# Kernel optimization log

Measured on AMD Instinct MI355X. Metric: run time of the kernel, lower is better.

The kernel has to match this reference:

```python
import jax, jax.numpy as jnp
import numpy as np

B, L, U, G, H = 64, 110, 768, 512, 256
WP = WF = 10
NSP = 2
R = 2 * NSP * NSP      # 8 relation types
NB = 30                # RGCN num_bases
FF = 2048              # torch TransformerEncoderLayer default dim_feedforward
TAG = 7
N = B * L
NEG = -1e9


def _build_edges():
    # static windowed edge structure (all dialogues have length L)
    js, ks = [], []
    for j in range(L):
        for k in range(max(0, j - WP), min(L - 1, j + WF) + 1):
            js.append(j); ks.append(k)
    j = np.asarray(js, np.int32); k = np.asarray(ks, np.int32)
    c = (j >= k).astype(np.int32)  # edge_type suffix: '0' if j<k else '1'
    off = (np.arange(B, dtype=np.int32) * L)[:, None]
    src = (j[None, :] + off).reshape(-1)
    dst = (k[None, :] + off).reshape(-1)
    return src, dst, np.tile(k, B), np.tile(c, B)


def _ln(x, g, b):
    m = x.mean(-1, keepdims=True)
    v = ((x - m) ** 2).mean(-1, keepdims=True)
    return (x - m) / jnp.sqrt(v + 1e-5) * g + b


def _core(x, in_proj_w, in_proj_b, out_proj_w, out_proj_b, ln1_g, ln1_b,
          ff1_w, ff1_b, ff2_w, ff2_b, ln2_g, ln2_b, to_w, to_b, att_w,
          rgcn_basis, rgcn_comp, rgcn_root, rgcn_bias,
          gc_rel_w, gc_rel_b, gc_root_w, clf1_w, clf1_b, clf2_w, clf2_b,
          speaker, src, dst, k_local, cflag):
    # --- SeqContext: 1-layer, 1-head post-norm transformer (eval mode) ---
    qkv = x @ in_proj_w.T + in_proj_b
    q, kk, v = jnp.split(qkv, 3, axis=-1)
    attn = jax.nn.softmax(jnp.einsum('bqd,bkd->bqk', q, kk) / jnp.sqrt(jnp.float32(U)), -1)
    a = jnp.einsum('bqk,bkd->bqd', attn, v) @ out_proj_w.T + out_proj_b
    h = _ln(x + a, ln1_g, ln1_b)
    ff = jax.nn.relu(h @ ff1_w.T + ff1_b) @ ff2_w.T + ff2_b
    h = _ln(h + ff, ln2_g, ln2_b)
    feats = h @ to_w.T + to_b                      # (B, L, G) node features

    # --- EdgeAtt: windowed softmax attention, score[j,k] = x_j^T W x_k ---
    scores = jnp.einsum('bjd,de,bke->bjk', feats, att_w, feats)
    rel = jnp.arange(L)[None, :] - jnp.arange(L)[:, None]
    mask = (rel >= -WP) & (rel <= WF)
    alpha = jax.nn.softmax(jnp.where(mask[None], scores, NEG), -1)  # (B, L, L)

    xf = feats.reshape(N, G)
    edge_norm = alpha.reshape(N, L)[src, k_local]   # alpha[b, j, k] per edge

    # --- edge types from speakers: idx = (s1*NSP + s2)*2 + c ---
    sp = speaker.reshape(N)
    etype = (sp[src] * NSP + sp[dst]) * 2 + cflag

    # --- RGCNConv: basis decomposition, per-(node, relation) mean + root ---
    w_rel = jnp.einsum('rb,bgh->rgh', rgcn_comp, rgcn_basis)   # (R, G, H)
    xproj = jnp.einsum('ng,rgh->rnh', xf, w_rel)               # (R, N, H)
    msg = xproj[etype, src]                                    # (E, H)
    seg = dst * R + etype
    cnt = jax.ops.segment_sum(jnp.ones_like(edge_norm), seg, num_segments=N * R)
    msg = msg / jnp.maximum(cnt[seg], 1.0)[:, None]
    h1 = jax.ops.segment_sum(msg, dst, num_segments=N) + xf @ rgcn_root + rgcn_bias

    # --- GraphConv: sum-aggregate edge-weighted neighbors + root ---
    agg = jax.ops.segment_sum(edge_norm[:, None] * h1[src], dst, num_segments=N)
    h2 = agg @ gc_rel_w.T + gc_rel_b + h1 @ gc_root_w.T

    # --- Classifier (dropout inactive in eval) ---
    z = jnp.concatenate([xf, h2], axis=-1)
    return jax.nn.relu(z @ clf1_w.T + clf1_b) @ clf2_w.T + clf2_b  # (N, TAG)


def setup_inputs():
    key = jax.random.key(0)
    ks = jax.random.split(key, 16)
    def rn(i, shape, scale=0.02):
        return jax.random.normal(ks[i], shape, jnp.float32) * scale
    src, dst, k_local, cflag = _build_edges()
    return {
        'x': jax.random.normal(ks[0], (B, L, U), jnp.float32),
        'in_proj_w': rn(1, (3 * U, U)), 'in_proj_b': jnp.zeros((3 * U,), jnp.float32),
        'out_proj_w': rn(2, (U, U)), 'out_proj_b': jnp.zeros((U,), jnp.float32),
        'ln1_g': jnp.ones((U,), jnp.float32), 'ln1_b': jnp.zeros((U,), jnp.float32),
        'ff1_w': rn(3, (FF, U)), 'ff1_b': jnp.zeros((FF,), jnp.float32),
        'ff2_w': rn(4, (U, FF)), 'ff2_b': jnp.zeros((U,), jnp.float32),
        'ln2_g': jnp.ones((U,), jnp.float32), 'ln2_b': jnp.zeros((U,), jnp.float32),
        'to_w': rn(5, (G, U)), 'to_b': jnp.zeros((G,), jnp.float32),
        'att_w': rn(6, (G, G), 2.0 / (G + G)),
        'rgcn_basis': rn(7, (NB, G, H)), 'rgcn_comp': rn(8, (R, NB), 0.2),
        'rgcn_root': rn(9, (G, H)), 'rgcn_bias': jnp.zeros((H,), jnp.float32),
        'gc_rel_w': rn(10, (H, H)), 'gc_rel_b': jnp.zeros((H,), jnp.float32),
        'gc_root_w': rn(11, (H, H)),
        'clf1_w': rn(12, (H, G + H)), 'clf1_b': jnp.zeros((H,), jnp.float32),
        'clf2_w': rn(13, (TAG, H)), 'clf2_b': jnp.zeros((TAG,), jnp.float32),
        'speaker': jax.random.randint(ks[14], (B, L), 0, NSP, jnp.int32),
        'src': jnp.asarray(src), 'dst': jnp.asarray(dst),
        'k_local': jnp.asarray(k_local), 'cflag': jnp.asarray(cflag),
        'length': L,
    }


def reference(x, in_proj_w, in_proj_b, out_proj_w, out_proj_b, ln1_g, ln1_b,
              ff1_w, ff1_b, ff2_w, ff2_b, ln2_g, ln2_b, to_w, to_b, att_w,
              rgcn_basis, rgcn_comp, rgcn_root, rgcn_bias,
              gc_rel_w, gc_rel_b, gc_root_w, clf1_w, clf1_b, clf2_w, clf2_b,
              speaker, src, dst, k_local, cflag, length):
    return _core(x, in_proj_w, in_proj_b, out_proj_w, out_proj_b, ln1_g, ln1_b,
                 ff1_w, ff1_b, ff2_w, ff2_b, ln2_g, ln2_b, to_w, to_b, att_w,
                 rgcn_basis, rgcn_comp, rgcn_root, rgcn_bias,
                 gc_rel_w, gc_rel_b, gc_root_w, clf1_w, clf1_b, clf2_w, clf2_b,
                 speaker, src, dst, k_local, cflag)
```

## Files before the change

### kernel.cpp

```cpp
#include <hip/hip_runtime.h>
#include <hip/hip_bf16.h>
#include <math.h>

#define L_   110
#define B_   64
#define N_   7040
#define U_   768
#define G_   512
#define H_   256
#define FF_  2048
#define EPB_ 2200
#define NC_  2816

typedef __attribute__((ext_vector_type(4))) float f32x4;
typedef __attribute__((ext_vector_type(8))) short bf16x8;

__device__ __forceinline__ ushort f2b(float f) {
  union { __hip_bfloat16 h; ushort u; } cv;
  cv.h = __float2bfloat16(f);
  return cv.u;
}
__device__ __forceinline__ float b2f(ushort u) {
  union { float f; unsigned int i; } cv; cv.i = ((unsigned int)u) << 16; return cv.f;
}

__device__ __forceinline__ int edge_prefix(int j) {
  if (j <= 10)  return j * 11 + (j * (j - 1)) / 2;
  if (j <= 100) return 155 + (j - 10) * 21;
  return 2045 + ((141 - j) * (j - 100)) / 2;
}

struct Segs7 { const float* in[7]; ushort* out[7]; int n4[7]; };

__global__ __launch_bounds__(256)
void cvtmulti_kernel(Segs7 s)
{
  const int seg = blockIdx.y;
  const int n4 = s.n4[seg];
  const float* __restrict__ in = s.in[seg];
  ushort* __restrict__ out = s.out[seg];
  for (int i = blockIdx.x * 256 + threadIdx.x; i < n4; i += gridDim.x * 256) {
    float4 v = ((const float4*)in)[i];
    ushort4 o;
    o.x = f2b(v.x); o.y = f2b(v.y); o.z = f2b(v.z); o.w = f2b(v.w);
    ((ushort4*)out)[i] = o;
  }
}

__global__ __launch_bounds__(256)
void tcvt_kernel(const float* __restrict__ in, ushort* __restrict__ out,
                 int R, int C, size_t inStride, size_t outStride)
{
  __shared__ float t[32][33];
  const int bt = blockIdx.z;
  const int r0 = blockIdx.y * 32, c0 = blockIdx.x * 32;
  const int tx = threadIdx.x & 31, ty = threadIdx.x >> 5;
  for (int i = ty; i < 32; i += 8)
    t[i][tx] = in[bt * inStride + (size_t)(r0 + i) * C + c0 + tx];
  __syncthreads();
  for (int i = ty; i < 32; i += 8)
    out[bt * outStride + (size_t)(c0 + i) * R + r0 + tx] = f2b(t[tx][i]);
}

__global__ __launch_bounds__(256)
void wrel_kernel(const float* __restrict__ basis, const float* __restrict__ comp,
                 float* __restrict__ wrel)
{
  __shared__ float cs[240];
  const int tid = threadIdx.x;
  if (tid < 240) cs[tid] = comp[tid];
  __syncthreads();
  const int gh = blockIdx.x * 256 + tid;
  float acc[8] = {};
  for (int bb = 0; bb < 30; ++bb) {
    float v = basis[(size_t)bb * (G_ * H_) + gh];
#pragma unroll
    for (int r = 0; r < 8; ++r) acc[r] = fmaf(cs[r * 30 + bb], v, acc[r]);
  }
#pragma unroll
  for (int r = 0; r < 8; ++r) wrel[(size_t)r * (G_ * H_) + gh] = acc[r];
}

__global__ void biascomb_kernel(const float* __restrict__ rb, float* __restrict__ bias)
{
  int i = blockIdx.x * 256 + threadIdx.x;
  if (i < NC_) bias[i] = (i < 2560) ? 0.f : rb[i - 2560];
}

__global__ __launch_bounds__(256)
void gccat_kernel(const float* __restrict__ rel, const float* __restrict__ root,
                  ushort* __restrict__ outp)
{
  int i = blockIdx.x * 256 + threadIdx.x;
  const int r = i >> 8, c = i & 255;
  outp[(size_t)r * 512 + c]       = f2b(rel[i]);
  outp[(size_t)r * 512 + 256 + c] = f2b(root[i]);
}

template<bool BIAS, bool RELU, bool ACC, bool OUTF, bool OUTB>
__global__ __launch_bounds__(256)
void mgemm_kernel(const ushort* __restrict__ A, const ushort* __restrict__ B,
                  const float* __restrict__ bias, const float* __restrict__ Cin,
                  float* __restrict__ Cf, ushort* __restrict__ Cb,
                  int K, int lda, int ldb, int ldc)
{
  __shared__ ushort sA[128 * 64];
  __shared__ ushort sB[128 * 64];
  const int tid = threadIdx.x;
  const int w = tid >> 6, l = tid & 63;

  const int gx = gridDim.x;
  const int nwg = gx * gridDim.y;
  const int lid = blockIdx.y * gx + blockIdx.x;
  const int q = nwg >> 3, r = nwg & 7;
  const int xcd = lid & 7, pos = lid >> 3;
  const int nlid = (xcd < r ? xcd * (q + 1) : r * (q + 1) + (xcd - r) * q) + pos;
  const int m0 = (nlid / gx) * 128, n0 = (nlid % gx) * 128;

  const int srow = l >> 3, sg = l & 7, rbase = w * 32;
  const int wr = w >> 1, wc = w & 1;
  const int lrow = l & 15, lk = l >> 4;
  const int xm = (l & 7) << 4;
  const int kb0 = (lk * 16) ^ xm;
  int aoff[4], boff[4];
#pragma unroll
  for (int i = 0; i < 4; ++i) {
    aoff[i] = (wr * 64 + i * 16 + lrow) * 128 + kb0;
    boff[i] = (wc * 64 + i * 16 + lrow) * 128 + kb0;
  }

  f32x4 acc[4][4];
#pragma unroll
  for (int i = 0; i < 4; ++i)
#pragma unroll
    for (int j = 0; j < 4; ++j) acc[i][j] = (f32x4){0.f, 0.f, 0.f, 0.f};

#define STAGE(k0)                                                              \
  {                                                                            \
    _Pragma("unroll")                                                          \
    for (int i = 0; i < 4; ++i) {                                              \
      const int trow = rbase + i * 8 + srow;                                   \
      const int koff = (sg * 8) ^ ((trow & 7) << 3);                           \
      const ushort* ga = A + (size_t)(m0 + trow) * lda + (k0) + koff;          \
      const ushort* gb = B + (size_t)(n0 + trow) * ldb + (k0) + koff;          \
      __builtin_amdgcn_global_load_lds(                                        \
          (const __attribute__((address_space(1))) void*)ga,                   \
          (__attribute__((address_space(3))) void*)&sA[(rbase + i * 8) * 64],  \
          16, 0, 0);                                                           \
      __builtin_amdgcn_global_load_lds(                                        \
          (const __attribute__((address_space(1))) void*)gb,                   \
          (__attribute__((address_space(3))) void*)&sB[(rbase + i * 8) * 64],  \
          16, 0, 0);                                                           \
    }                                                                          \
  }

  STAGE(0)
  for (int kt = 0;;) {
    __syncthreads();
#pragma unroll
    for (int h = 0; h < 2; ++h) {
      const int hx = h * 64;
      bf16x8 af[4], bfr[4];
#pragma unroll
      for (int i = 0; i < 4; ++i) {
        af[i]  = *(const bf16x8*)&sA[(aoff[i] ^ hx) >> 1];
        bfr[i] = *(const bf16x8*)&sB[(boff[i] ^ hx) >> 1];
      }
#pragma unroll
      for (int mi = 0; mi < 4; ++mi)
#pragma unroll
        for (int ni = 0; ni < 4; ++ni)
          acc[mi][ni] = __builtin_amdgcn_mfma_f32_16x16x32_bf16(
              af[mi], bfr[ni], acc[mi][ni], 0, 0, 0);
    }
    kt += 64;
    if (kt >= K) break;
    __syncthreads();
    STAGE(kt)
  }
#undef STAGE

  const int orow = m0 + wr * 64 + lk * 4;
  const int ocol = n0 + wc * 64 + lrow;
#pragma unroll
  for (int mi = 0; mi < 4; ++mi) {
#pragma unroll
    for (int r2 = 0; r2 < 4; ++r2) {
      const int row = orow + mi * 16 + r2;
#pragma unroll
      for (int ni = 0; ni < 4; ++ni) {
        const int col = ocol + ni * 16;
        float v = acc[mi][ni][r2];
        if constexpr (ACC)  v += Cin[(size_t)row * ldc + col];
        if constexpr (BIAS) v += bias[col];
        if constexpr (RELU) v = fmaxf(v, 0.f);
        if constexpr (OUTF) Cf[(size_t)row * ldc + col] = v;
        if constexpr (OUTB) Cb[(size_t)row * ldc + col] = f2b(v);
      }
    }
  }
}

__global__ __launch_bounds__(256)
void vtrans_kernel(const ushort* __restrict__ qkvb, ushort* __restrict__ vt)
{
  __shared__ ushort t[32][33];
  const int b = blockIdx.z;
  const int r0 = blockIdx.y * 32;
  const int c0 = blockIdx.x * 32;
  const int tx = threadIdx.x & 31, ty = threadIdx.x >> 5;
  for (int i = ty; i < 32; i += 8) {
    const int r = r0 + i;
    t[i][tx] = (r < L_) ? qkvb[((size_t)(b * L_) + r) * 2304 + 1536 + c0 + tx]
                        : (ushort)0;
  }
  __syncthreads();
  for (int i = ty; i < 32; i += 8)
    vt[((size_t)b * 768 + c0 + i) * 128 + r0 + tx] = t[tx][i];
}

__global__ __launch_bounds__(256)
void attnM_kernel(const ushort* __restrict__ qkvb, const ushort* __restrict__ vt,
                  ushort* __restrict__ ctxb)
{
  const int wg = blockIdx.x;
  const int xcd = wg & 7, slot = wg >> 3;
  const int b = xcd * 8 + slot / 7;
  const int qr0 = (slot % 7) * 16;
  const int tid = threadIdx.x, w = tid >> 6, l = tid & 63;
  __shared__ float  sS[16 * 128];
  __shared__ ushort sP[16 * 128];
  const int lrow = l & 15, lq = l >> 4;

  const ushort* Qbase = qkvb + ((size_t)(b * L_) + qr0 + lrow) * 2304 + lq * 8;
  f32x4 accS[2] = {{0.f,0.f,0.f,0.f},{0.f,0.f,0.f,0.f}};
  const int nf0 = w * 2;
  for (int k0 = 0; k0 < 768; k0 += 32) {
    bf16x8 aq = *(const bf16x8*)(Qbase + k0);
#pragma unroll
    for (int f = 0; f < 2; ++f) {
      const int nf = nf0 + f;
      if (nf < 7) {
        const ushort* Kp = qkvb + ((size_t)(b * L_) + nf * 16 + lrow) * 2304
                         + 768 + k0 + lq * 8;
        bf16x8 bk = *(const bf16x8*)Kp;
        accS[f] = __builtin_amdgcn_mfma_f32_16x16x32_bf16(aq, bk, accS[f], 0, 0, 0);
      }
    }
  }
  const float scale = 0.03608439182435161f;
#pragma unroll
  for (int f = 0; f < 2; ++f) {
    const int nf = nf0 + f;
    if (nf < 7) {
#pragma unroll
      for (int r = 0; r < 4; ++r)
        sS[(lq * 4 + r) * 128 + nf * 16 + lrow] = accS[f][r] * scale;
    }
  }
  __syncthreads();

  {
    const int row = w * 4 + lq;
    const int c0 = lrow;
    float m = -1e30f;
    for (int c = c0; c < L_; c += 16) m = fmaxf(m, sS[row * 128 + c]);
#pragma unroll
    for (int off = 8; off; off >>= 1) m = fmaxf(m, __shfl_xor(m, off));
    float pv[7];
    float sum = 0.f;
#pragma unroll
    for (int i = 0; i < 7; ++i) {
      const int c = c0 + i * 16;
      float e = (c < L_) ? __expf(sS[row * 128 + c] - m) : 0.f;
      pv[i] = e; sum += e;
    }
#pragma unroll
    for (int off = 8; off; off >>= 1) sum += __shfl_xor(sum, off);
    const float inv = 1.f / sum;
#pragma unroll
    for (int i = 0; i < 8; ++i) {
      const int c = c0 + i * 16;
      ushort pb = (i < 7 && c < L_) ? f2b(pv[i < 7 ? i : 0] * inv) : (ushort)0;
      const int g = (c >> 3) ^ (row & 7);
      sP[row * 128 + g * 8 + (c & 7)] = pb;
    }
  }
  __syncthreads();

  f32x4 accO[12];
#pragma unroll
  for (int i = 0; i < 12; ++i) accO[i] = (f32x4){0.f, 0.f, 0.f, 0.f};
#pragma unroll
  for (int ks = 0; ks < 4; ++ks) {
    const int k = ks * 32 + lq * 8;
    const int g = (k >> 3) ^ (lrow & 7);
    bf16x8 ap = *(const bf16x8*)&sP[lrow * 128 + g * 8];
#pragma unroll
    for (int i = 0; i < 12; ++i) {
      const int col = w * 192 + i * 16 + lrow;
      bf16x8 bv = *(const bf16x8*)(vt + ((size_t)b * 768 + col) * 128 + k);
      accO[i] = __builtin_amdgcn_mfma_f32_16x16x32_bf16(ap, bv, accO[i], 0, 0, 0);
    }
  }
#pragma unroll
  for (int i = 0; i < 12; ++i) {
    const int col = w * 192 + i * 16 + lrow;
#pragma unroll
    for (int r = 0; r < 4; ++r) {
      const int row = qr0 + lq * 4 + r;
      if (row < L_)
        ctxb[((size_t)b * L_ + row) * 768 + col] = f2b(accO[i][r]);
    }
  }
}

__global__ __launch_bounds__(256)
void ln_kernel(const float* __restrict__ A, const float* __restrict__ Bres,
               const float* __restrict__ g, const float* __restrict__ beta,
               float* __restrict__ out, ushort* __restrict__ outb)
{
  const int row = blockIdx.x, tid = threadIdx.x;
  const float* ap = A + (size_t)row * U_;
  const float* bp = Bres + (size_t)row * U_;
  float v0 = ap[tid] + bp[tid];
  float v1 = ap[tid + 256] + bp[tid + 256];
  float v2 = ap[tid + 512] + bp[tid + 512];
  float s = v0 + v1 + v2, sq = v0 * v0 + v1 * v1 + v2 * v2;
  __shared__ float red[8];
#pragma unroll
  for (int off = 32; off; off >>= 1) { s += __shfl_xor(s, off); sq += __shfl_xor(sq, off); }
  const int wave = tid >> 6, lane = tid & 63;
  if (lane == 0) { red[wave] = s; red[4 + wave] = sq; }
  __syncthreads();
  if (tid == 0) {
    float ts = red[0] + red[1] + red[2] + red[3];
    float tq = red[4] + red[5] + red[6] + red[7];
    float m = ts * (1.f / 768.f);
    float var = tq * (1.f / 768.f) - m * m;
    red[0] = m; red[1] = 1.f / sqrtf(var + 1e-5f);
  }
  __syncthreads();
  const float m = red[0], inv = red[1];
  float* op = out + (size_t)row * U_;
  ushort* ob = outb + (size_t)row * U_;
  float o0 = (v0 - m) * inv * g[tid] + beta[tid];
  float o1 = (v1 - m) * inv * g[tid + 256] + beta[tid + 256];
  float o2 = (v2 - m) * inv * g[tid + 512] + beta[tid + 512];
  op[tid] = o0; op[tid + 256] = o1; op[tid + 512] = o2;
  ob[tid] = f2b(o0); ob[tid + 256] = f2b(o1); ob[tid + 512] = f2b(o2);
}

__global__ __launch_bounds__(256)
void edgeatt_kernel(const ushort* __restrict__ tmpB, const ushort* __restrict__ fcat,
                    float* __restrict__ edge_norm)
{
  const int bj = blockIdx.x;
  const int b = bj / L_, j = bj - b * L_;
  const int k0 = max(0, j - 10), k1 = min(L_ - 1, j + 10);
  __shared__ float s[32];
  const int tid = threadIdx.x;
  const int wave = tid >> 6, lane = tid & 63;
  const ushort* tp = tmpB + (size_t)bj * NC_ + lane * 8;
  float tr[8];
  {
    bf16x8 tv = *(const bf16x8*)tp;
#pragma unroll
    for (int i = 0; i < 8; ++i) tr[i] = b2f((ushort)tv[i]);
  }
  for (int k = k0 + wave; k <= k1; k += 4) {
    const ushort* fp = fcat + (size_t)(b * L_ + k) * 768 + lane * 8;
    bf16x8 v = *(const bf16x8*)fp;
    float sc = 0.f;
#pragma unroll
    for (int i = 0; i < 8; ++i) sc = fmaf(b2f((ushort)v[i]), tr[i], sc);
#pragma unroll
    for (int off = 32; off; off >>= 1) sc += __shfl_xor(sc, off);
    if (lane == 0) s[k - k0] = sc;
  }
  __syncthreads();
  if (tid == 0) {
    const int W = k1 - k0 + 1;
    float m = -1e30f;
    for (int t = 0; t < W; ++t) m = fmaxf(m, s[t]);
    float sum = 0.f;
    for (int t = 0; t < W; ++t) { float e = __expf(s[t] - m); s[t] = e; sum += e; }
    const float inv = 1.f / sum;
    const int base = b * EPB_ + edge_prefix(j);
    for (int t = 0; t < W; ++t) edge_norm[base + t] = s[t] * inv;
  }
}

__global__ __launch_bounds__(256)
void rgcn_gather2_kernel(const ushort* __restrict__ xcomb,
                         const int* __restrict__ speaker,
                         ushort* __restrict__ catb)
{
  const int tid = threadIdx.x;
  const int n = blockIdx.x * 8 + (tid >> 5);
  const int lane = tid & 31;
  const int b = n / L_, k = n - b * L_;
  const int j0 = max(0, k - 10), j1 = min(L_ - 1, k + 10);
  const int spk = speaker[n];
  float inv[4];
  {
    int cn[4] = {0, 0, 0, 0};
    for (int j = j0; j <= j1; ++j)
      cn[speaker[b * L_ + j] * 2 + (j >= k ? 1 : 0)]++;
#pragma unroll
    for (int q = 0; q < 4; ++q) inv[q] = cn[q] ? 1.f / (float)cn[q] : 0.f;
  }
  float acc[8] = {};
  for (int j = j0; j <= j1; ++j) {
    const int spj = speaker[b * L_ + j];
    const int c = (j >= k) ? 1 : 0;
    const int et = (spj * 2 + spk) * 2 + c;
    const float w = inv[spj * 2 + c];
    bf16x8 v = *(const bf16x8*)&xcomb[(size_t)(b * L_ + j) * NC_ + 512 + et * 256 + lane * 8];
#pragma unroll
    for (int i = 0; i < 8; ++i) acc[i] = fmaf(b2f((ushort)v[i]), w, acc[i]);
  }
  bf16x8 rt = *(const bf16x8*)&xcomb[(size_t)n * NC_ + 2560 + lane * 8];
  bf16x8 o;
#pragma unroll
  for (int i = 0; i < 8; ++i) o[i] = (short)f2b(acc[i] + b2f((ushort)rt[i]));
  *(bf16x8*)&catb[(size_t)n * 512 + 256 + lane * 8] = o;
}

__global__ __launch_bounds__(256)
void gcn_gather2_kernel(const float* __restrict__ edge_norm,
                        ushort* __restrict__ catb)
{
  const int tid = threadIdx.x;
  const int n = blockIdx.x * 8 + (tid >> 5);
  const int lane = tid & 31;
  const int b = n / L_, k = n - b * L_;
  const int j0 = max(0, k - 10), j1 = min(L_ - 1, k + 10);
  float acc[8] = {};
  for (int j = j0; j <= j1; ++j) {
    const float w = edge_norm[b * EPB_ + edge_prefix(j) + (k - max(0, j - 10))];
    bf16x8 v = *(const bf16x8*)&catb[(size_t)(b * L_ + j) * 512 + 256 + lane * 8];
#pragma unroll
    for (int i = 0; i < 8; ++i) acc[i] = fmaf(b2f((ushort)v[i]), w, acc[i]);
  }
  bf16x8 o;
#pragma unroll
  for (int i = 0; i < 8; ++i) o[i] = (short)f2b(acc[i]);
  *(bf16x8*)&catb[(size_t)n * 512 + lane * 8] = o;
}

__global__ __launch_bounds__(256)
void clf2_kernel(const float* __restrict__ hid, const float* __restrict__ w,
                 const float* __restrict__ bias, float* __restrict__ out)
{
  __shared__ float wsm[7 * H_];
  const int tid = threadIdx.x;
  for (int i = tid; i < 7 * H_; i += 256) wsm[i] = w[i];
  __syncthreads();
  const int idx = blockIdx.x * 256 + threadIdx.x;
  if (idx < N_ * 7) {
    const int n = idx / 7, t = idx - n * 7;
    const float* hp = hid + (size_t)n * H_;
    const float* wp = wsm + t * H_;
    float acc = bias[t];
    for (int d = 0; d < H_; ++d) acc = fmaf(hp[d], wp[d], acc);
    out[idx] = acc;
  }
}

extern "C" void kernel_launch(void* const* d_in, const int* in_sizes, int n_in,
                              void* d_out, int out_size, void* d_ws, size_t ws_size,
                              hipStream_t stream)
{
  const float* x          = (const float*)d_in[0];
  const float* in_proj_w  = (const float*)d_in[1];
  const float* in_proj_b  = (const float*)d_in[2];
  const float* out_proj_w = (const float*)d_in[3];
  const float* out_proj_b = (const float*)d_in[4];
  const float* ln1_g      = (const float*)d_in[5];
  const float* ln1_b      = (const float*)d_in[6];
  const float* ff1_w      = (const float*)d_in[7];
  const float* ff1_b      = (const float*)d_in[8];
  const float* ff2_w      = (const float*)d_in[9];
  const float* ff2_b      = (const float*)d_in[10];
  const float* ln2_g      = (const float*)d_in[11];
  const float* ln2_b      = (const float*)d_in[12];
  const float* to_w       = (const float*)d_in[13];
  const float* to_b       = (const float*)d_in[14];
  const float* att_w      = (const float*)d_in[15];
  const float* rgcn_basis = (const float*)d_in[16];
  const float* rgcn_comp  = (const float*)d_in[17];
  const float* rgcn_root  = (const float*)d_in[18];
  const float* rgcn_bias  = (const float*)d_in[19];
  const float* gc_rel_w   = (const float*)d_in[20];
  const float* gc_rel_b   = (const float*)d_in[21];
  const float* gc_root_w  = (const float*)d_in[22];
  const float* clf1_w     = (const float*)d_in[23];
  const float* clf1_b     = (const float*)d_in[24];
  const float* clf2_w     = (const float*)d_in[25];
  const float* clf2_b     = (const float*)d_in[26];
  const int*   speaker    = (const int*)d_in[27];
  float* out = (float*)d_out;
  char* p = (char*)d_ws;

  float*  R1f    = (float*)p;
  ushort* R1b    = (ushort*)p;
  p += (size_t)N_ * 2304 * 4;
  float*  aproj = (float*)p;
  float*  ffo   = aproj;
  float*  en    = (float*)(p + (size_t)N_ * 512 * 4);
  p += (size_t)N_ * 768 * 4;
  float*  hbuf  = (float*)p;
  ushort* vt    = (ushort*)p;
  float*  hid   = (float*)p;
  p += (size_t)N_ * 768 * 4;
  ushort* xb    = (ushort*)p;
  ushort* ctxb  = xb;
  p += (size_t)N_ * 768 * 2;
  ushort* hb    = (ushort*)p;
  ushort* catb  = hb;
  p += (size_t)N_ * 768 * 2;
  ushort* fcat  = (ushort*)p; p += (size_t)N_ * 768 * 2;
  ushort* in_projb = (ushort*)p; p += (size_t)2304 * 768 * 2;
  ushort* out_projb= (ushort*)p; p += (size_t)768 * 768 * 2;
  ushort* ff1b     = (ushort*)p; p += (size_t)2048 * 768 * 2;
  ushort* ff2b     = (ushort*)p; p += (size_t)768 * 2048 * 2;
  ushort* tob      = (ushort*)p; p += (size_t)512 * 768 * 2;
  ushort* combw    = (ushort*)p; p += (size_t)NC_ * 512 * 2;
  ushort* gccat    = (ushort*)p; p += (size_t)256 * 512 * 2;
  ushort* clf1b16  = (ushort*)p; p += (size_t)256 * 768 * 2;
  float*  bias_comb= (float*)p;  p += NC_ * 4;
  float*  wrelTmp  = R1f;

  Segs7 segs;
  segs.in[0] = x;          segs.out[0] = xb;        segs.n4[0] = N_ * 768 / 4;
  segs.in[1] = in_proj_w;  segs.out[1] = in_projb;  segs.n4[1] = 2304 * 768 / 4;
  segs.in[2] = out_proj_w; segs.out[2] = out_projb; segs.n4[2] = 768 * 768 / 4;
  segs.in[3] = ff1_w;      segs.out[3] = ff1b;      segs.n4[3] = 2048 * 768 / 4;
  segs.in[4] = ff2_w;      segs.out[4] = ff2b;      segs.n4[4] = 768 * 2048 / 4;
  segs.in[5] = to_w;       segs.out[5] = tob;       segs.n4[5] = 512 * 768 / 4;
  segs.in[6] = clf1_w;     segs.out[6] = clf1b16;   segs.n4[6] = 256 * 768 / 4;
  cvtmulti_kernel<<<dim3(768, 7), 256, 0, stream>>>(segs);
  gccat_kernel<<<256, 256, 0, stream>>>(gc_rel_w, gc_root_w, gccat);
  tcvt_kernel<<<dim3(16, 16, 1), 256, 0, stream>>>(att_w, combw, 512, 512, 0, 0);
  wrel_kernel<<<512, 256, 0, stream>>>(rgcn_basis, rgcn_comp, wrelTmp);
  tcvt_kernel<<<dim3(8, 16, 8), 256, 0, stream>>>(wrelTmp, combw + (size_t)512 * 512,
                                                  512, 256,
                                                  (size_t)512 * 256, (size_t)256 * 512);
  tcvt_kernel<<<dim3(8, 16, 1), 256, 0, stream>>>(rgcn_root, combw + (size_t)2560 * 512,
                                                  512, 256, 0, 0);
  biascomb_kernel<<<11, 256, 0, stream>>>(rgcn_bias, bias_comb);

  mgemm_kernel<true, false, false, false, true><<<dim3(18, 55), 256, 0, stream>>>(
      xb, in_projb, in_proj_b, nullptr, nullptr, R1b, 768, 768, 768, 2304);
  vtrans_kernel<<<dim3(24, 4, 64), 256, 0, stream>>>(R1b, vt);
  attnM_kernel<<<448, 256, 0, stream>>>(R1b, vt, ctxb);
  mgemm_kernel<true, false, false, true, false><<<dim3(6, 55), 256, 0, stream>>>(
      ctxb, out_projb, out_proj_b, nullptr, aproj, nullptr, 768, 768, 768, 768);
  ln_kernel<<<N_, 256, 0, stream>>>(x, aproj, ln1_g, ln1_b, hbuf, hb);
  mgemm_kernel<true, true, false, false, true><<<dim3(16, 55), 256, 0, stream>>>(
      hb, ff1b, ff1_b, nullptr, nullptr, R1b, 768, 768, 768, 2048);
  mgemm_kernel<true, false, false, true, false><<<dim3(6, 55), 256, 0, stream>>>(
      R1b, ff2b, ff2_b, nullptr, ffo, nullptr, 2048, 2048, 2048, 768);
  ln_kernel<<<N_, 256, 0, stream>>>(hbuf, ffo, ln2_g, ln2_b, hbuf, hb);
  mgemm_kernel<true, false, false, false, true><<<dim3(4, 55), 256, 0, stream>>>(
      hb, tob, to_b, nullptr, nullptr, fcat, 768, 768, 768, 768);
  mgemm_kernel<true, false, false, false, true><<<dim3(22, 55), 256, 0, stream>>>(
      fcat, combw, bias_comb, nullptr, nullptr, R1b, 512, 768, 512, NC_);
  edgeatt_kernel<<<N_, 256, 0, stream>>>(R1b, fcat, en);
  rgcn_gather2_kernel<<<N_ / 8, 256, 0, stream>>>(R1b, speaker, catb);
  gcn_gather2_kernel<<<N_ / 8, 256, 0, stream>>>(en, catb);
  mgemm_kernel<true, false, false, false, true><<<dim3(2, 55), 256, 0, stream>>>(
      catb, gccat, gc_rel_b, nullptr, nullptr, fcat + 512, 512, 512, 512, 768);
  mgemm_kernel<true, true, false, true, false><<<dim3(2, 55), 256, 0, stream>>>(
      fcat, clf1b16, clf1_b, nullptr, hid, nullptr, 768, 768, 768, 256);
  clf2_kernel<<<(N_ * 7 + 255) / 256, 256, 0, stream>>>(hid, clf2_w, clf2_b, out);
}
```

Measured before the change: 349.3 us.

## Fuse V-transpose into QKV GEMM, merge small kernels, switch intermediates to bf16

Several independent changes are combined. The V transpose is folded into the QKV GEMM epilogue, and the bias-combine, gccat and vt-padding-zero kernels are merged into one prep kernel. The edge-attention and RGCN gather kernels are merged into one launch, and GEMM outputs feeding LayerNorm and clf2 are stored as bf16 instead of fp32. The aim is to cut launch count and memory traffic, at the cost of more rounding error and strided scattered writes for the transposed V.

New measurement: 337.1 us. -3.5%, faster.

```diff
diff --git a/kernel.cpp b/kernel.cpp
--- a/kernel.cpp
+++ b/kernel.cpp
@@ -81,27 +81,31 @@
   for (int r = 0; r < 8; ++r) wrel[(size_t)r * (G_ * H_) + gh] = acc[r];
 }
 
-__global__ void biascomb_kernel(const float* __restrict__ rb, float* __restrict__ bias)
-{
-  int i = blockIdx.x * 256 + threadIdx.x;
-  if (i < NC_) bias[i] = (i < 2560) ? 0.f : rb[i - 2560];
-}
-
-__global__ __launch_bounds__(256)
-void gccat_kernel(const float* __restrict__ rel, const float* __restrict__ root,
-                  ushort* __restrict__ outp)
-{
-  int i = blockIdx.x * 256 + threadIdx.x;
-  const int r = i >> 8, c = i & 255;
-  outp[(size_t)r * 512 + c]       = f2b(rel[i]);
-  outp[(size_t)r * 512 + 256 + c] = f2b(root[i]);
-}
-
-template<bool BIAS, bool RELU, bool ACC, bool OUTF, bool OUTB>
+__global__ __launch_bounds__(256)
+void prepmisc_kernel(const float* __restrict__ rb, const float* __restrict__ rel,
+                     const float* __restrict__ root, float* __restrict__ bias,
+                     ushort* __restrict__ gccat, ushort* __restrict__ vt)
+{
+  const int i = blockIdx.x * 256 + threadIdx.x;
+  if (i < NC_) {
+    bias[i] = (i < 2560) ? 0.f : rb[i - 2560];
+  } else if (i < NC_ + 65536) {
+    const int j = i - NC_;
+    const int r = j >> 8, c = j & 255;
+    gccat[(size_t)r * 512 + c]       = f2b(rel[j]);
+    gccat[(size_t)r * 512 + 256 + c] = f2b(root[j]);
+  } else if (i < NC_ + 65536 + 64 * 768 * 18) {
+    const int j = i - (NC_ + 65536);
+    const int bd = j / 18, kk = 110 + (j - bd * 18);
+    vt[(size_t)bd * 128 + kk] = 0;
+  }
+}
+
+template<bool BIAS, bool RELU, bool OUTB, bool VTOUT>
 __global__ __launch_bounds__(256)
 void mgemm_kernel(const ushort* __restrict__ A, const ushort* __restrict__ B,
-                  const float* __restrict__ bias, const float* __restrict__ Cin,
-                  float* __restrict__ Cf, ushort* __restrict__ Cb,
+                  const float* __restrict__ bias, ushort* __restrict__ Cb,
+                  ushort* __restrict__ Vt,
                   int K, int lda, int ldb, int ldc)
 {
   __shared__ ushort sA[128 * 64];
@@ -191,32 +195,19 @@
       for (int ni = 0; ni < 4; ++ni) {
         const int col = ocol + ni * 16;
         float v = acc[mi][ni][r2];
-        if constexpr (ACC)  v += Cin[(size_t)row * ldc + col];
         if constexpr (BIAS) v += bias[col];
         if constexpr (RELU) v = fmaxf(v, 0.f);
-        if constexpr (OUTF) Cf[(size_t)row * ldc + col] = v;
-        if constexpr (OUTB) Cb[(size_t)row * ldc + col] = f2b(v);
+        const ushort vb = f2b(v);
+        if constexpr (OUTB) Cb[(size_t)row * ldc + col] = vb;
+        if constexpr (VTOUT) {
+          if (col >= 1536) {
+            const int brow = row / L_, kk = row - brow * L_;
+            Vt[((size_t)brow * 768 + (col - 1536)) * 128 + kk] = vb;
+          }
+        }
       }
     }
   }
-}
-
-__global__ __launch_bounds__(256)
-void vtrans_kernel(const ushort* __restrict__ qkvb, ushort* __restrict__ vt)
-{
-  __shared__ ushort t[32][33];
-  const int b = blockIdx.z;
-  const int r0 = blockIdx.y * 32;
-  const int c0 = blockIdx.x * 32;
-  const int tx = threadIdx.x & 31, ty = threadIdx.x >> 5;
-  for (int i = ty; i < 32; i += 8) {
-    const int r = r0 + i;
-    t[i][tx] = (r < L_) ? qkvb[((size_t)(b * L_) + r) * 2304 + 1536 + c0 + tx]
-                        : (ushort)0;
-  }
-  __syncthreads();
-  for (int i = ty; i < 32; i += 8)
-    vt[((size_t)b * 768 + c0 + i) * 128 + r0 + tx] = t[tx][i];
 }
 
 __global__ __launch_bounds__(256)
@@ -315,17 +306,18 @@
   }
 }
 
-__global__ __launch_bounds__(256)
-void ln_kernel(const float* __restrict__ A, const float* __restrict__ Bres,
+template<bool WF>
+__global__ __launch_bounds__(256)
+void ln_kernel(const float* __restrict__ A, const ushort* __restrict__ Bres,
                const float* __restrict__ g, const float* __restrict__ beta,
                float* __restrict__ out, ushort* __restrict__ outb)
 {
   const int row = blockIdx.x, tid = threadIdx.x;
   const float* ap = A + (size_t)row * U_;
-  const float* bp = Bres + (size_t)row * U_;
-  float v0 = ap[tid] + bp[tid];
-  float v1 = ap[tid + 256] + bp[tid + 256];
-  float v2 = ap[tid + 512] + bp[tid + 512];
+  const ushort* bp = Bres + (size_t)row * U_;
+  float v0 = ap[tid] + b2f(bp[tid]);
+  float v1 = ap[tid + 256] + b2f(bp[tid + 256]);
+  float v2 = ap[tid + 512] + b2f(bp[tid + 512]);
   float s = v0 + v1 + v2, sq = v0 * v0 + v1 * v1 + v2 * v2;
   __shared__ float red[8];
 #pragma unroll
@@ -342,89 +334,85 @@
   }
   __syncthreads();
   const float m = red[0], inv = red[1];
-  float* op = out + (size_t)row * U_;
   ushort* ob = outb + (size_t)row * U_;
   float o0 = (v0 - m) * inv * g[tid] + beta[tid];
   float o1 = (v1 - m) * inv * g[tid + 256] + beta[tid + 256];
   float o2 = (v2 - m) * inv * g[tid + 512] + beta[tid + 512];
-  op[tid] = o0; op[tid + 256] = o1; op[tid + 512] = o2;
+  if constexpr (WF) {
+    float* op = out + (size_t)row * U_;
+    op[tid] = o0; op[tid + 256] = o1; op[tid + 512] = o2;
+  }
   ob[tid] = f2b(o0); ob[tid + 256] = f2b(o1); ob[tid + 512] = f2b(o2);
 }
 
 __global__ __launch_bounds__(256)
-void edgeatt_kernel(const ushort* __restrict__ tmpB, const ushort* __restrict__ fcat,
-                    float* __restrict__ edge_norm)
-{
-  const int bj = blockIdx.x;
-  const int b = bj / L_, j = bj - b * L_;
-  const int k0 = max(0, j - 10), k1 = min(L_ - 1, j + 10);
-  __shared__ float s[32];
+void graphfront_kernel(const ushort* __restrict__ combo, const ushort* __restrict__ fcat,
+                       const int* __restrict__ speaker,
+                       ushort* __restrict__ catb, float* __restrict__ edge_norm)
+{
   const int tid = threadIdx.x;
-  const int wave = tid >> 6, lane = tid & 63;
-  const ushort* tp = tmpB + (size_t)bj * NC_ + lane * 8;
-  float tr[8];
-  {
-    bf16x8 tv = *(const bf16x8*)tp;
-#pragma unroll
-    for (int i = 0; i < 8; ++i) tr[i] = b2f((ushort)tv[i]);
-  }
-  for (int k = k0 + wave; k <= k1; k += 4) {
-    const ushort* fp = fcat + (size_t)(b * L_ + k) * 768 + lane * 8;
-    bf16x8 v = *(const bf16x8*)fp;
-    float sc = 0.f;
-#pragma unroll
-    for (int i = 0; i < 8; ++i) sc = fmaf(b2f((ushort)v[i]), tr[i], sc);
-#pragma unroll
-    for (int off = 32; off; off >>= 1) sc += __shfl_xor(sc, off);
-    if (lane == 0) s[k - k0] = sc;
-  }
-  __syncthreads();
-  if (tid == 0) {
-    const int W = k1 - k0 + 1;
-    float m = -1e30f;
-    for (int t = 0; t < W; ++t) m = fmaxf(m, s[t]);
-    float sum = 0.f;
-    for (int t = 0; t < W; ++t) { float e = __expf(s[t] - m); s[t] = e; sum += e; }
-    const float inv = 1.f / sum;
-    const int base = b * EPB_ + edge_prefix(j);
-    for (int t = 0; t < W; ++t) edge_norm[base + t] = s[t] * inv;
-  }
-}
-
-__global__ __launch_bounds__(256)
-void rgcn_gather2_kernel(const ushort* __restrict__ xcomb,
-                         const int* __restrict__ speaker,
-                         ushort* __restrict__ catb)
-{
-  const int tid = threadIdx.x;
-  const int n = blockIdx.x * 8 + (tid >> 5);
-  const int lane = tid & 31;
-  const int b = n / L_, k = n - b * L_;
-  const int j0 = max(0, k - 10), j1 = min(L_ - 1, k + 10);
-  const int spk = speaker[n];
-  float inv[4];
-  {
-    int cn[4] = {0, 0, 0, 0};
-    for (int j = j0; j <= j1; ++j)
-      cn[speaker[b * L_ + j] * 2 + (j >= k ? 1 : 0)]++;
-#pragma unroll
-    for (int q = 0; q < 4; ++q) inv[q] = cn[q] ? 1.f / (float)cn[q] : 0.f;
-  }
-  float acc[8] = {};
-  for (int j = j0; j <= j1; ++j) {
-    const int spj = speaker[b * L_ + j];
-    const int c = (j >= k) ? 1 : 0;
-    const int et = (spj * 2 + spk) * 2 + c;
-    const float w = inv[spj * 2 + c];
-    bf16x8 v = *(const bf16x8*)&xcomb[(size_t)(b * L_ + j) * NC_ + 512 + et * 256 + lane * 8];
-#pragma unroll
-    for (int i = 0; i < 8; ++i) acc[i] = fmaf(b2f((ushort)v[i]), w, acc[i]);
-  }
-  bf16x8 rt = *(const bf16x8*)&xcomb[(size_t)n * NC_ + 2560 + lane * 8];
-  bf16x8 o;
-#pragma unroll
-  for (int i = 0; i < 8; ++i) o[i] = (short)f2b(acc[i] + b2f((ushort)rt[i]));
-  *(bf16x8*)&catb[(size_t)n * 512 + 256 + lane * 8] = o;
+  if (blockIdx.x < N_ / 8) {
+    const int n = blockIdx.x * 8 + (tid >> 5);
+    const int lane = tid & 31;
+    const int b = n / L_, k = n - b * L_;
+    const int j0 = max(0, k - 10), j1 = min(L_ - 1, k + 10);
+    const int spk = speaker[n];
+    float inv[4];
+    {
+      int cn[4] = {0, 0, 0, 0};
+      for (int j = j0; j <= j1; ++j)
+        cn[speaker[b * L_ + j] * 2 + (j >= k ? 1 : 0)]++;
+#pragma unroll
+      for (int q = 0; q < 4; ++q) inv[q] = cn[q] ? 1.f / (float)cn[q] : 0.f;
+    }
+    float acc[8] = {};
+    for (int j = j0; j <= j1; ++j) {
+      const int spj = speaker[b * L_ + j];
+      const int c = (j >= k) ? 1 : 0;
+      const int et = (spj * 2 + spk) * 2 + c;
+      const float w = inv[spj * 2 + c];
+      bf16x8 v = *(const bf16x8*)&combo[(size_t)(b * L_ + j) * NC_ + 512 + et * 256 + lane * 8];
+#pragma unroll
+      for (int i = 0; i < 8; ++i) acc[i] = fmaf(b2f((ushort)v[i]), w, acc[i]);
+    }
+    bf16x8 rt = *(const bf16x8*)&combo[(size_t)n * NC_ + 2560 + lane * 8];
+    bf16x8 o;
+#pragma unroll
+    for (int i = 0; i < 8; ++i) o[i] = (short)f2b(acc[i] + b2f((ushort)rt[i]));
+    *(bf16x8*)&catb[(size_t)n * 512 + 256 + lane * 8] = o;
+  } else {
+    const int bj = blockIdx.x - N_ / 8;
+    const int b = bj / L_, j = bj - b * L_;
+    const int k0 = max(0, j - 10), k1 = min(L_ - 1, j + 10);
+    __shared__ float s[32];
+    const int wave = tid >> 6, lane = tid & 63;
+    float tr[8];
+    {
+      bf16x8 tv = *(const bf16x8*)&combo[(size_t)bj * NC_ + lane * 8];
+#pragma unroll
+      for (int i = 0; i < 8; ++i) tr[i] = b2f((ushort)tv[i]);
+    }
+    for (int k = k0 + wave; k <= k1; k += 4) {
+      bf16x8 v = *(const bf16x8*)&fcat[(size_t)(b * L_ + k) * 768 + lane * 8];
+      float sc = 0.f;
+#pragma unroll
+      for (int i = 0; i < 8; ++i) sc = fmaf(b2f((ushort)v[i]), tr[i], sc);
+#pragma unroll
+      for (int off = 32; off; off >>= 1) sc += __shfl_xor(sc, off);
+      if (lane == 0) s[k - k0] = sc;
+    }
+    __syncthreads();
+    if (tid == 0) {
+      const int W = k1 - k0 + 1;
+      float m = -1e30f;
+      for (int t = 0; t < W; ++t) m = fmaxf(m, s[t]);
+      float sum = 0.f;
+      for (int t = 0; t < W; ++t) { float e = __expf(s[t] - m); s[t] = e; sum += e; }
+      const float inv = 1.f / sum;
+      const int base = b * EPB_ + edge_prefix(j);
+      for (int t = 0; t < W; ++t) edge_norm[base + t] = s[t] * inv;
+    }
+  }
 }
 
 __global__ __launch_bounds__(256)
@@ -450,7 +438,7 @@
 }
 
 __global__ __launch_bounds__(256)
-void clf2_kernel(const float* __restrict__ hid, const float* __restrict__ w,
+void clf2_kernel(const ushort* __restrict__ hid, const float* __restrict__ w,
                  const float* __restrict__ bias, float* __restrict__ out)
 {
   __shared__ float wsm[7 * H_];
@@ -460,10 +448,14 @@
   const int idx = blockIdx.x * 256 + threadIdx.x;
   if (idx < N_ * 7) {
     const int n = idx / 7, t = idx - n * 7;
-    const float* hp = hid + (size_t)n * H_;
+    const ushort* hp = hid + (size_t)n * H_;
     const float* wp = wsm + t * H_;
     float acc = bias[t];
-    for (int d = 0; d < H_; ++d) acc = fmaf(hp[d], wp[d], acc);
+    for (int d0 = 0; d0 < H_; d0 += 8) {
+      bf16x8 v = *(const bf16x8*)(hp + d0);
+#pragma unroll
+      for (int i = 0; i < 8; ++i) acc = fmaf(b2f((ushort)v[i]), wp[d0 + i], acc);
+    }
     out[idx] = acc;
   }
 }
@@ -506,13 +498,13 @@
   float*  R1f    = (float*)p;
   ushort* R1b    = (ushort*)p;
   p += (size_t)N_ * 2304 * 4;
-  float*  aproj = (float*)p;
-  float*  ffo   = aproj;
-  float*  en    = (float*)(p + (size_t)N_ * 512 * 4);
+  ushort* aprojB = (ushort*)p;
+  ushort* ffoB   = aprojB;
+  float*  en     = (float*)(p + (size_t)N_ * 512 * 4);
   p += (size_t)N_ * 768 * 4;
   float*  hbuf  = (float*)p;
   ushort* vt    = (ushort*)p;
-  float*  hid   = (float*)p;
+  ushort* hidB  = (ushort*)p;
   p += (size_t)N_ * 768 * 4;
   ushort* xb    = (ushort*)p;
   ushort* ctxb  = xb;
@@ -541,7 +533,8 @@
   segs.in[5] = to_w;       segs.out[5] = tob;       segs.n4[5] = 512 * 768 / 4;
   segs.in[6] = clf1_w;     segs.out[6] = clf1b16;   segs.n4[6] = 256 * 768 / 4;
   cvtmulti_kernel<<<dim3(768, 7), 256, 0, stream>>>(segs);
-  gccat_kernel<<<256, 256, 0, stream>>>(gc_rel_w, gc_root_w, gccat);
+  prepmisc_kernel<<<(NC_ + 65536 + 64 * 768 * 18 + 255) / 256, 256, 0, stream>>>(
+      rgcn_bias, gc_rel_w, gc_root_w, bias_comb, gccat, vt);
   tcvt_kernel<<<dim3(16, 16, 1), 256, 0, stream>>>(att_w, combw, 512, 512, 0, 0);
   wrel_kernel<<<512, 256, 0, stream>>>(rgcn_basis, rgcn_comp, wrelTmp);
   tcvt_kernel<<<dim3(8, 16, 8), 256, 0, stream>>>(wrelTmp, combw + (size_t)512 * 512,
@@ -549,30 +542,27 @@
                                                   (size_t)512 * 256, (size_t)256 * 512);
   tcvt_kernel<<<dim3(8, 16, 1), 256, 0, stream>>>(rgcn_root, combw + (size_t)2560 * 512,
                                                   512, 256, 0, 0);
-  biascomb_kernel<<<11, 256, 0, stream>>>(rgcn_bias, bias_comb);
-
-  mgemm_kernel<true, false, false, false, true><<<dim3(18, 55), 256, 0, stream>>>(
-      xb, in_projb, in_proj_b, nullptr, nullptr, R1b, 768, 768, 768, 2304);
-  vtrans_kernel<<<dim3(24, 4, 64), 256, 0, stream>>>(R1b, vt);
+
+  mgemm_kernel<true, false, true, true><<<dim3(18, 55), 256, 0, stream>>>(
+      xb, in_projb, in_proj_b, R1b, vt, 768, 768, 768, 2304);
   attnM_kernel<<<448, 256, 0, stream>>>(R1b, vt, ctxb);
-  mgemm_kernel<true, false, false, true, false><<<dim3(6, 55), 256, 0, stream>>>(
-      ctxb, out_projb, out_proj_b, nullptr, aproj, nullptr, 768, 768, 768, 768);
-  ln_kernel<<<N_, 256, 0, stream>>>(x, aproj, ln1_g, ln1_b, hbuf, hb);
-  mgemm_kernel<true, true, false, false, true><<<dim3(16, 55), 256, 0, stream>>>(
-      hb, ff1b, ff1_b, nullptr, nullptr, R1b, 768, 768, 768, 2048);
-  mgemm_kernel<true, false, false, true, false><<<dim3(6, 55), 256, 0, stream>>>(
-      R1b, ff2b, ff2_b, nullptr, ffo, nullptr, 2048, 2048, 2048, 768);
-  ln_kernel<<<N_, 256, 0, stream>>>(hbuf, ffo, ln2_g, ln2_b, hbuf, hb);
-  mgemm_kernel<true, false, false, false, true><<<dim3(4, 55), 256, 0, stream>>>(
-      hb, tob, to_b, nullptr, nullptr, fcat, 768, 768, 768, 768);
-  mgemm_kernel<true, false, false, false, true><<<dim3(22, 55), 256, 0, stream>>>(
-      fcat, combw, bias_comb, nullptr, nullptr, R1b, 512, 768, 512, NC_);
-  edgeatt_kernel<<<N_, 256, 0, stream>>>(R1b, fcat, en);
-  rgcn_gather2_kernel<<<N_ / 8, 256, 0, stream>>>(R1b, speaker, catb);
+  mgemm_kernel<true, false, true, false><<<dim3(6, 55), 256, 0, stream>>>(
+      ctxb, out_projb, out_proj_b, aprojB, nullptr, 768, 768, 768, 768);
+  ln_kernel<true><<<N_, 256, 0, stream>>>(x, aprojB, ln1_g, ln1_b, hbuf, hb);
+  mgemm_kernel<true, true, true, false><<<dim3(16, 55), 256, 0, stream>>>(
+      hb, ff1b, ff1_b, R1b, nullptr, 768, 768, 768, 2048);
+  mgemm_kernel<true, false, true, false><<<dim3(6, 55), 256, 0, stream>>>(
+      R1b, ff2b, ff2_b, ffoB, nullptr, 2048, 2048, 2048, 768);
+  ln_kernel<false><<<N_, 256, 0, stream>>>(hbuf, ffoB, ln2_g, ln2_b, nullptr, hb);
+  mgemm_kernel<true, false, true, false><<<dim3(4, 55), 256, 0, stream>>>(
+      hb, tob, to_b, fcat, nullptr, 768, 768, 768, 768);
+  mgemm_kernel<true, false, true, false><<<dim3(22, 55), 256, 0, stream>>>(
+      fcat, combw, bias_comb, R1b, nullptr, 512, 768, 512, NC_);
+  graphfront_kernel<<<N_ / 8 + N_, 256, 0, stream>>>(R1b, fcat, speaker, catb, en);
   gcn_gather2_kernel<<<N_ / 8, 256, 0, stream>>>(en, catb);
-  mgemm_kernel<true, false, false, false, true><<<dim3(2, 55), 256, 0, stream>>>(
-      catb, gccat, gc_rel_b, nullptr, nullptr, fcat + 512, 512, 512, 512, 768);
-  mgemm_kernel<true, true, false, true, false><<<dim3(2, 55), 256, 0, stream>>>(
-      fcat, clf1b16, clf1_b, nullptr, hid, nullptr, 768, 768, 768, 256);
-  clf2_kernel<<<(N_ * 7 + 255) / 256, 256, 0, stream>>>(hid, clf2_w, clf2_b, out);
-}
+  mgemm_kernel<true, false, true, false><<<dim3(2, 55), 256, 0, stream>>>(
+      catb, gccat, gc_rel_b, fcat + 512, nullptr, 512, 512, 512, 768);
+  mgemm_kernel<true, true, true, false><<<dim3(2, 55), 256, 0, stream>>>(
+      fcat, clf1b16, clf1_b, hidB, nullptr, 768, 768, 768, 256);
+  clf2_kernel<<<(N_ * 7 + 255) / 256, 256, 0, stream>>>(hidB, clf2_w, clf2_b, out);
+}
```
